# Kernel optimization log

Measured on AMD Instinct MI355X. Metric: run time of the kernel, lower is better.

The kernel has to match this reference:

```python
import jax, jax.numpy as jnp
import numpy as np

FS = 16000
NUM_BANDS = 15
CENTER_FREQ = 150
FFT_SIZE = 512
FFT_IN = 256
HOP = 128
NUM_FRAMES = 30
BETA = 1.0 + 10.0 ** (15.0 / 20.0)
FFT_PAD = (FFT_SIZE - FFT_IN) // 2
ROWS = FFT_SIZE // 2 + 1


def _make_fftmat():
    window = np.hanning(FFT_IN)
    window = np.concatenate([np.zeros(FFT_PAD), window, np.zeros(FFT_PAD)])
    fft = np.fft.fft(np.eye(FFT_SIZE))
    fft = np.vstack((np.real(fft[:ROWS, :]), np.imag(fft[:ROWS, :])))
    fft = window * fft  # (2*ROWS, FFT_SIZE)
    return fft.astype(np.float32)


def _make_octmat(fs=FS, nfft=FFT_SIZE, numBands=NUM_BANDS, mn=CENTER_FREQ):
    f = np.linspace(0, fs, nfft + 1)
    f = f[: int(nfft / 2) + 1]
    k = np.arange(float(numBands))
    cf = 2 ** (k / 3) * mn
    fl = np.sqrt(2.0 ** (k / 3) * mn * 2 ** ((k - 1.0) / 3) * mn)
    fr = np.sqrt(2.0 ** (k / 3) * mn * 2 ** ((k + 1.0) / 3) * mn)
    A = np.zeros((numBands, len(f)))
    for i in range(len(cf)):
        b = np.argmin((f - fl[i]) ** 2)
        fl[i] = f[b]
        fl_ii = b
        b = np.argmin((f - fr[i]) ** 2)
        fr[i] = f[b]
        fr_ii = b
        A[i, np.arange(fl_ii, fr_ii)] = 1
    rnk = np.sum(A, axis=1)
    nb = np.where((rnk[1:] >= rnk[:-1]) & (rnk[1:] != 0))[-1][-1] + 1
    A = A[: nb + 1, :]
    return A.astype(np.float32)


def setup_inputs() -> dict:
    key = jax.random.key(0)
    k1, k2, k3 = jax.random.split(key, 3)
    B, L = 64, 128000
    return {
        "prediction": jax.random.normal(k1, (B, L), dtype=jnp.float32),
        "target": jax.random.normal(k2, (B, L), dtype=jnp.float32),
        "inteference": jax.random.normal(k3, (B, L), dtype=jnp.float32),
        "fftmat": jnp.asarray(_make_fftmat()),   # (514, 512)
        "octmat": jnp.asarray(_make_octmat()),   # (n_bands, 257)
    }


def _stft_mag(seq, fftmat):
    # seq: (B, L) -> conv1d with stride HOP, padding FFT_PAD
    out = jax.lax.conv_general_dilated(
        seq[:, None, :], fftmat[:, None, :],
        window_strides=(HOP,), padding=[(FFT_PAD, FFT_PAD)],
        dimension_numbers=("NCH", "OIH", "NCH"))
    real, imag = out[:, :ROWS, :], out[:, ROWS:, :]
    return jnp.sqrt(real ** 2 + imag ** 2)  # (B, ROWS, T)


def _stoi_loss(prediction, target, fftmat, octmat):
    pred_mag = _stft_mag(prediction, fftmat)
    targ_mag = _stft_mag(target, fftmat)
    # octave-band energies: (B, n_bands, T)
    x = jnp.sqrt(jnp.einsum("bft,kf->bkt", targ_mag ** 2, octmat))
    y = jnp.sqrt(jnp.einsum("bft,kf->bkt", pred_mag ** 2, octmat))
    T = x.shape[2]
    W = T - NUM_FRAMES  # windows for m in [NUM_FRAMES, T)
    idx = jnp.arange(W)[:, None] + jnp.arange(NUM_FRAMES)[None, :]  # (W, 30)
    xw = x[:, :, idx]  # (B, K, W, 30)
    yw = y[:, :, idx]
    alpha = jnp.sqrt(jnp.sum(xw ** 2, axis=3, keepdims=True)
                     / (jnp.sum(yw ** 2, axis=3, keepdims=True) + 1e-07))
    yp = jnp.minimum(alpha * yw, BETA * xw)
    xn = xw - jnp.mean(xw, axis=3, keepdims=True)
    xn = xn / jnp.sqrt(jnp.sum(xn ** 2, axis=3, keepdims=True))
    yn = yp - jnp.mean(yp, axis=3, keepdims=True)
    yn = yn / jnp.sqrt(jnp.sum(yn ** 2, axis=3, keepdims=True))
    # per-window correlation: mean over (B, K) of sum over time
    r = jnp.mean(jnp.sum(xn * yn, axis=3), axis=(0, 1))  # (W,)
    return -jnp.sum(r) / W


def reference(prediction, target, inteference, fftmat, octmat):
    return _stoi_loss(prediction, target, fftmat, octmat)
```

## Files before the change

### kernel.cpp

```cpp
#include <hip/hip_runtime.h>
#include <math.h>

#define SIG_L 128000
#define NBATCH 64
#define NROWS 257
#define HOP 128
#define NUMF 999
#define NFRM 30
#define NWIN 969
#define NB_MAX 16
#define FBINS 160
#define TILES 9
#define KSTEPS 16
#define FPBX 256
#define NTX 4
#define AKB 18432
#define BCH 4112
#define BETA_F 6.623413251903491f

typedef __attribute__((ext_vector_type(8))) short short8;
typedef __attribute__((ext_vector_type(16))) float f32x16;
typedef unsigned short ushort_t;

__device__ inline ushort_t bf_hi_rne(float v, float* rem) {
    unsigned u = __float_as_uint(v);
    unsigned hr = (u + 0x7FFFu + ((u >> 16) & 1u)) & 0xFFFF0000u;
    *rem = v - __uint_as_float(hr);
    return (ushort_t)(hr >> 16);
}
__device__ inline ushort_t bf_rne(float v) {
    unsigned u = __float_as_uint(v);
    return (ushort_t)((u + 0x7FFFu + ((u >> 16) & 1u)) >> 16);
}

__device__ inline void gll16(const void* g, void* l) {
    __builtin_amdgcn_global_load_lds(
        (const __attribute__((address_space(1))) unsigned int*)g,
        (__attribute__((address_space(3))) unsigned int*)l, 16, 0, 0);
}

__global__ void k_scan(const float* __restrict__ oct, int NB, int* __restrict__ hdr) {
    __shared__ int smin[16], smax[16];
    int tid = threadIdx.x;
    if (tid < NB) { smin[tid] = 0x7fffffff; smax[tid] = -1; }
    __syncthreads();
    for (int idx = tid; idx < NB * NROWS; idx += blockDim.x) {
        int k = idx / NROWS, f = idx % NROWS;
        if (oct[idx] != 0.0f) { atomicMin(&smin[k], f); atomicMax(&smax[k], f); }
    }
    __syncthreads();
    if (tid < FBINS) {
        int kid = -1;
        for (int k = 0; k < NB; ++k)
            if (smax[k] >= 0 && tid >= smin[k] && tid <= smax[k]) kid = k;
        hdr[32 + tid] = kid;
    }
}

__global__ void k_prep(const float* __restrict__ fftmat, ushort_t* __restrict__ wpack) {
    for (int u = 0; u < 2; ++u) {
        int idx = blockIdx.x * 512 + u * 256 + threadIdx.x;
        int e = idx & 7, l = (idx >> 3) & 63, p = (idx >> 9) & 1;
        int tt = (idx >> 10) % TILES, kk = (idx >> 10) / TILES;
        int row32 = l & 31, kq = l >> 5;
        int bin = tt * 16 + (row32 >> 1);
        int part = row32 & 1;
        int k = kk * 16 + kq * 8 + e;
        float v = fftmat[(size_t)(part ? (NROWS + bin) : bin) * 512 + 128 + k];
        float rem; ushort_t hb = bf_hi_rne(v, &rem);
        wpack[idx] = p ? bf_rne(rem) : hb;
    }
}

__global__ __launch_bounds__(768, 3) void k_stft(
    const float* __restrict__ targ, const float* __restrict__ pred,
    const ushort_t* __restrict__ wpack, const int* __restrict__ hdr,
    float* __restrict__ xbuf, float* __restrict__ ybuf, int NB) {
    __shared__ __align__(16) char smem[2 * AKB + BCH * 16 + NB_MAX * FPBX * 4 + 640];
    ushort_t* As    = (ushort_t*)smem;
    char*     Bs    = smem + 2 * AKB;
    float*    bacc  = (float*)(smem + 2 * AKB + BCH * 16);
    int*      kmapS = (int*)(smem + 2 * AKB + BCH * 16 + NB_MAX * FPBX * 4);

    const int tid = threadIdx.x;
    const int lane = tid & 63;
    const int wv = __builtin_amdgcn_readfirstlane(tid >> 6);
    const int mg  = wv >> 2;
    const int col = wv & 3;
    const int tbase = mg * 3;
    const int b = blockIdx.y, z = blockIdx.z;
    const int t0 = blockIdx.x * FPBX;
    const float* __restrict__ sig = z ? pred : targ;
    float* __restrict__ out = z ? ybuf : xbuf;
    const size_t boff = (size_t)b * SIG_L;

    for (int i = tid; i < NB_MAX * FPBX; i += 768) bacc[i] = 0.0f;
    for (int i = tid; i < FBINS; i += 768) kmapS[i] = hdr[32 + i];

    const long sbase = (long)t0 * HOP;
    for (int c = tid; c < BCH; c += 768) {
        const long g0 = sbase + (long)c * 8;
        float v[8];
        if (g0 + 8 <= SIG_L) {
            float4 x0 = *(const float4*)(sig + boff + g0);
            float4 x1 = *(const float4*)(sig + boff + g0 + 4);
            v[0] = x0.x; v[1] = x0.y; v[2] = x0.z; v[3] = x0.w;
            v[4] = x1.x; v[5] = x1.y; v[6] = x1.z; v[7] = x1.w;
        } else {
#pragma unroll
            for (int e = 0; e < 8; ++e)
                v[e] = (g0 + e < SIG_L) ? sig[boff + g0 + e] : 0.0f;
        }
        short8 sv;
#pragma unroll
        for (int e = 0; e < 8; ++e) sv[e] = (short)bf_rne(v[e]);
        int byte = c * 16;
        byte ^= ((byte >> 8) & 0xF) << 4;
        *(short8*)(Bs + byte) = sv;
    }
    {
        const char* gsrc = (const char*)wpack;
        for (int j = wv; j < 18; j += 12)
            gll16(gsrc + j * 1024 + lane * 16, smem + j * 1024);
    }
    __syncthreads();

    f32x16 acc[3][2];
#pragma unroll
    for (int g = 0; g < 3; ++g)
#pragma unroll
        for (int bt = 0; bt < 2; ++bt)
#pragma unroll
            for (int e = 0; e < 16; ++e) acc[g][bt][e] = 0.0f;

    const int jloc = lane & 31, kq = lane >> 5;

    int cur = 0;
#pragma unroll 1
    for (int kk = 0; kk < KSTEPS; ++kk) {
        if (kk < KSTEPS - 1) {
            const char* gsrc = (const char*)wpack + (size_t)(kk + 1) * AKB;
            char* ldst = smem + (cur ^ 1) * AKB;
            for (int j = wv; j < 18; j += 12)
                gll16(gsrc + j * 1024 + lane * 16, ldst + j * 1024);
        }
        short8 S[2];
#pragma unroll
        for (int bt = 0; bt < 2; ++bt) {
            const int fl = col * 64 + bt * 32 + jloc;
            int byte = fl * 256 + kk * 32 + kq * 16;
            byte ^= ((byte >> 8) & 0xF) << 4;
            S[bt] = *(const short8*)(Bs + byte);
        }
        const ushort_t* ab = As + cur * (AKB / 2) + tbase * 1024 + lane * 8;
        __builtin_amdgcn_s_setprio(1);
#pragma unroll
        for (int g = 0; g < 3; ++g) {
            short8 Ah = *(const short8*)(ab + g * 1024);
            short8 Al = *(const short8*)(ab + g * 1024 + 512);
            acc[g][0] = __builtin_amdgcn_mfma_f32_32x32x16_bf16(Ah, S[0], acc[g][0], 0, 0, 0);
            acc[g][1] = __builtin_amdgcn_mfma_f32_32x32x16_bf16(Ah, S[1], acc[g][1], 0, 0, 0);
            acc[g][0] = __builtin_amdgcn_mfma_f32_32x32x16_bf16(Al, S[0], acc[g][0], 0, 0, 0);
            acc[g][1] = __builtin_amdgcn_mfma_f32_32x32x16_bf16(Al, S[1], acc[g][1], 0, 0, 0);
        }
        __builtin_amdgcn_s_setprio(0);
        __syncthreads();
        cur ^= 1;
    }

#pragma unroll
    for (int g = 0; g < 3; ++g) {
#pragma unroll
        for (int bt = 0; bt < 2; ++bt) {
            const int fl = col * 64 + bt * 32 + jloc;
            float run = 0.0f; int runk = -1;
#pragma unroll
            for (int rr = 0; rr < 8; ++rr) {
                const int m = (rr & 1) + 4 * (rr >> 1) + 2 * kq;
                const int kid = kmapS[(tbase + g) * 16 + m];
                const float vr = acc[g][bt][rr * 2], vi = acc[g][bt][rr * 2 + 1];
                const float e = vr * vr + vi * vi;
                if (kid != runk) {
                    if (runk >= 0) atomicAdd(&bacc[runk * FPBX + fl], run);
                    run = 0.0f; runk = kid;
                }
                if (kid >= 0) run += e;
            }
            if (runk >= 0) atomicAdd(&bacc[runk * FPBX + fl], run);
        }
    }
    __syncthreads();
    for (int idx = tid; idx < NB * FPBX; idx += 768) {
        int k = idx >> 8, t = idx & (FPBX - 1);
        int tg = t0 + t;
        if (tg < NUMF)
            out[((size_t)b * NB + k) * NUMF + tg] = bacc[k * FPBX + t];
    }
}

__global__ __launch_bounds__(256) void k_corr(const float* __restrict__ xbuf,
                                              const float* __restrict__ ybuf,
                                              int NB, double* __restrict__ partials) {
    const int k = blockIdx.x, b = blockIdx.y;
    const long roff = ((long)b * NB + k) * NUMF;
    __shared__ float xl[NUMF], yl[NUMF];
    __shared__ double red[256];
    const int tid = threadIdx.x;
    for (int i = tid; i < NUMF; i += 256) {
        xl[i] = sqrtf(xbuf[roff + i]);
        yl[i] = sqrtf(ybuf[roff + i]);
    }
    __syncthreads();
    double loc = 0.0;
    for (int w = tid; w < NWIN; w += 256) {
        float sx = 0, sxx = 0, syy = 0;
        for (int i = 0; i < NFRM; ++i) {
            float xv = xl[w + i], yv = yl[w + i];
            sx += xv; sxx += xv * xv; syy += yv * yv;
        }
        float alpha = sqrtf(sxx / (syy + 1e-7f));
        float sy = 0;
        for (int i = 0; i < NFRM; ++i)
            sy += fminf(alpha * yl[w + i], BETA_F * xl[w + i]);
        float mx = sx * (1.0f / NFRM), my = sy * (1.0f / NFRM);
        float cxx = 0, cyy = 0, cxy = 0;
        for (int i = 0; i < NFRM; ++i) {
            float dx = xl[w + i] - mx;
            float dy = fminf(alpha * yl[w + i], BETA_F * xl[w + i]) - my;
            cxx += dx * dx; cyy += dy * dy; cxy += dx * dy;
        }
        loc += (double)cxy / sqrt((double)cxx * (double)cyy);
    }
    red[tid] = loc;
    __syncthreads();
    for (int s = 128; s > 0; s >>= 1) {
        if (tid < s) red[tid] += red[tid + s];
        __syncthreads();
    }
    if (tid == 0) partials[b * NB + k] = red[0];
}

__global__ void k_final(const double* __restrict__ partials, int NB, float* __restrict__ out) {
    __shared__ double red[256];
    const int tid = threadIdx.x;
    const int n = NBATCH * NB;
    double s = 0.0;
    for (int i = tid; i < n; i += 256) s += partials[i];
    red[tid] = s;
    __syncthreads();
    for (int st = 128; st > 0; st >>= 1) {
        if (tid < st) red[tid] += red[tid + st];
        __syncthreads();
    }
    if (tid == 0) out[0] = (float)(-red[0] / ((double)NBATCH * NB * NWIN));
}

extern "C" void kernel_launch(void* const* d_in, const int* in_sizes, int n_in,
                              void* d_out, int out_size, void* d_ws, size_t ws_size,
                              hipStream_t stream) {
    const float* pred   = (const float*)d_in[0];
    const float* targ   = (const float*)d_in[1];
    const float* fftmat = (const float*)d_in[3];
    const float* oct    = (const float*)d_in[4];
    const int NB = in_sizes[4] / NROWS;

    char* ws = (char*)d_ws;
    int*      hdr   = (int*)ws;
    ushort_t* wpack = (ushort_t*)(ws + 1024);
    size_t o1 = 1024 + (size_t)KSTEPS * TILES * 2 * 512 * 2;
    size_t xsz = (size_t)NBATCH * NB_MAX * NUMF * 4;
    float*  xbuf = (float*)(ws + o1);
    float*  ybuf = (float*)(ws + o1 + xsz);
    double* partials = (double*)(ws + o1 + 2 * xsz);

    hipLaunchKernelGGL(k_scan, dim3(1), dim3(256), 0, stream, oct, NB, hdr);
    hipLaunchKernelGGL(k_prep, dim3(288), dim3(256), 0, stream, fftmat, wpack);
    hipLaunchKernelGGL(k_stft, dim3(NTX, NBATCH, 2), dim3(768), 0, stream,
                       targ, pred, wpack, hdr, xbuf, ybuf, NB);
    hipLaunchKernelGGL(k_corr, dim3(NB, NBATCH), dim3(256), 0, stream, xbuf, ybuf, NB, partials);
    hipLaunchKernelGGL(k_final, dim3(1), dim3(256), 0, stream, partials, NB, (float*)d_out);
}
```

Baseline: 103.7 us.

## Make STFT kernel persistent over 256 blocks with batched signal loads

Turns k_stft from a 512-block grid into a 256-block grid where each block loops over two (tile, batch, signal) tasks. It also issues all global signal loads into registers before converting them to bf16, so the loads overlap. A new k_probe kernel with the same shared-memory footprint is launched before k_stft and does no useful work; it looks like a warm-up or timing experiment. The probe adds a launch and extra time to the measured sequence, and halving the block count may reduce parallelism on the device.

```diff
diff --git a/kernel.cpp b/kernel.cpp
--- a/kernel.cpp
+++ b/kernel.cpp
@@ -13,9 +13,9 @@
 #define TILES 9
 #define KSTEPS 16
 #define FPBX 256
-#define NTX 4
 #define AKB 18432
 #define BCH 4112
+#define SMEMSZ (2 * AKB + BCH * 16 + NB_MAX * FPBX * 4 + 640)
 #define BETA_F 6.623413251903491f
 
 typedef __attribute__((ext_vector_type(8))) short short8;
@@ -72,11 +72,22 @@
     }
 }
 
+__global__ __launch_bounds__(768, 3) void k_probe(float* sink) {
+    __shared__ __align__(16) char smem[SMEMSZ];
+    float* bacc = (float*)smem;
+    const int tid = threadIdx.x;
+    for (int i = tid; i < 4096; i += 768) bacc[i] = 0.0f;
+    __syncthreads();
+    float v = bacc[(tid * 37 + 1) & 4095];
+    asm volatile("" :: "v"(v));
+    (void)sink;
+}
+
 __global__ __launch_bounds__(768, 3) void k_stft(
     const float* __restrict__ targ, const float* __restrict__ pred,
     const ushort_t* __restrict__ wpack, const int* __restrict__ hdr,
     float* __restrict__ xbuf, float* __restrict__ ybuf, int NB) {
-    __shared__ __align__(16) char smem[2 * AKB + BCH * 16 + NB_MAX * FPBX * 4 + 640];
+    __shared__ __align__(16) char smem[SMEMSZ];
     ushort_t* As    = (ushort_t*)smem;
     char*     Bs    = smem + 2 * AKB;
     float*    bacc  = (float*)(smem + 2 * AKB + BCH * 16);
@@ -88,113 +99,126 @@
     const int mg  = wv >> 2;
     const int col = wv & 3;
     const int tbase = mg * 3;
-    const int b = blockIdx.y, z = blockIdx.z;
-    const int t0 = blockIdx.x * FPBX;
-    const float* __restrict__ sig = z ? pred : targ;
-    float* __restrict__ out = z ? ybuf : xbuf;
-    const size_t boff = (size_t)b * SIG_L;
-
-    for (int i = tid; i < NB_MAX * FPBX; i += 768) bacc[i] = 0.0f;
+    const int jloc = lane & 31, kq = lane >> 5;
+
     for (int i = tid; i < FBINS; i += 768) kmapS[i] = hdr[32 + i];
 
-    const long sbase = (long)t0 * HOP;
-    for (int c = tid; c < BCH; c += 768) {
-        const long g0 = sbase + (long)c * 8;
-        float v[8];
-        if (g0 + 8 <= SIG_L) {
-            float4 x0 = *(const float4*)(sig + boff + g0);
-            float4 x1 = *(const float4*)(sig + boff + g0 + 4);
-            v[0] = x0.x; v[1] = x0.y; v[2] = x0.z; v[3] = x0.w;
-            v[4] = x1.x; v[5] = x1.y; v[6] = x1.z; v[7] = x1.w;
-        } else {
-#pragma unroll
-            for (int e = 0; e < 8; ++e)
-                v[e] = (g0 + e < SIG_L) ? sig[boff + g0 + e] : 0.0f;
-        }
-        short8 sv;
-#pragma unroll
-        for (int e = 0; e < 8; ++e) sv[e] = (short)bf_rne(v[e]);
-        int byte = c * 16;
-        byte ^= ((byte >> 8) & 0xF) << 4;
-        *(short8*)(Bs + byte) = sv;
-    }
-    {
-        const char* gsrc = (const char*)wpack;
-        for (int j = wv; j < 18; j += 12)
-            gll16(gsrc + j * 1024 + lane * 16, smem + j * 1024);
-    }
-    __syncthreads();
-
-    f32x16 acc[3][2];
-#pragma unroll
-    for (int g = 0; g < 3; ++g)
-#pragma unroll
-        for (int bt = 0; bt < 2; ++bt)
-#pragma unroll
-            for (int e = 0; e < 16; ++e) acc[g][bt][e] = 0.0f;
-
-    const int jloc = lane & 31, kq = lane >> 5;
-
-    int cur = 0;
 #pragma unroll 1
-    for (int kk = 0; kk < KSTEPS; ++kk) {
-        if (kk < KSTEPS - 1) {
-            const char* gsrc = (const char*)wpack + (size_t)(kk + 1) * AKB;
-            char* ldst = smem + (cur ^ 1) * AKB;
+    for (int task = 0; task < 2; ++task) {
+        const int t = (int)blockIdx.x + 256 * task;
+        const int z = t & 1, b = (t >> 1) & 63, tile = (t >> 7) & 3;
+        const int t0 = tile * FPBX;
+        const float* __restrict__ sig = z ? pred : targ;
+        float* __restrict__ out = z ? ybuf : xbuf;
+        const size_t boff = (size_t)b * SIG_L;
+
+        if (task) __syncthreads();
+        for (int i = tid; i < NB_MAX * FPBX; i += 768) bacc[i] = 0.0f;
+
+        const long sbase = (long)t0 * HOP;
+        float4 xr[12];
+#pragma unroll
+        for (int u = 0; u < 6; ++u) {
+            const int c = tid + u * 768;
+            const long g0 = sbase + (long)c * 8;
+            const bool full = (c < BCH) && (g0 + 8 <= SIG_L);
+            const long gc = full ? g0 : 0;
+            const float* p = sig + boff + gc;
+            float4 a0 = *(const float4*)(p);
+            float4 a1 = *(const float4*)(p + 4);
+            if (!full) { a0 = (float4){0,0,0,0}; a1 = (float4){0,0,0,0}; }
+            xr[2*u] = a0; xr[2*u+1] = a1;
+        }
+#pragma unroll
+        for (int u = 0; u < 6; ++u) {
+            const int c = tid + u * 768;
+            if (c < BCH) {
+                short8 sv;
+                sv[0]=(short)bf_rne(xr[2*u].x);   sv[1]=(short)bf_rne(xr[2*u].y);
+                sv[2]=(short)bf_rne(xr[2*u].z);   sv[3]=(short)bf_rne(xr[2*u].w);
+                sv[4]=(short)bf_rne(xr[2*u+1].x); sv[5]=(short)bf_rne(xr[2*u+1].y);
+                sv[6]=(short)bf_rne(xr[2*u+1].z); sv[7]=(short)bf_rne(xr[2*u+1].w);
+                int byte = c * 16;
+                byte ^= ((byte >> 8) & 0xF) << 4;
+                *(short8*)(Bs + byte) = sv;
+            }
+        }
+        {
+            const char* gsrc = (const char*)wpack;
             for (int j = wv; j < 18; j += 12)
-                gll16(gsrc + j * 1024 + lane * 16, ldst + j * 1024);
-        }
-        short8 S[2];
-#pragma unroll
-        for (int bt = 0; bt < 2; ++bt) {
-            const int fl = col * 64 + bt * 32 + jloc;
-            int byte = fl * 256 + kk * 32 + kq * 16;
-            byte ^= ((byte >> 8) & 0xF) << 4;
-            S[bt] = *(const short8*)(Bs + byte);
-        }
-        const ushort_t* ab = As + cur * (AKB / 2) + tbase * 1024 + lane * 8;
-        __builtin_amdgcn_s_setprio(1);
+                gll16(gsrc + j * 1024 + lane * 16, smem + j * 1024);
+        }
+        __syncthreads();
+
+        f32x16 acc[3][2];
+#pragma unroll
+        for (int g = 0; g < 3; ++g)
+#pragma unroll
+            for (int bt = 0; bt < 2; ++bt)
+#pragma unroll
+                for (int e = 0; e < 16; ++e) acc[g][bt][e] = 0.0f;
+
+        int cur = 0;
+#pragma unroll 1
+        for (int kk = 0; kk < KSTEPS; ++kk) {
+            if (kk < KSTEPS - 1) {
+                const char* gsrc = (const char*)wpack + (size_t)(kk + 1) * AKB;
+                char* ldst = smem + (cur ^ 1) * AKB;
+                for (int j = wv; j < 18; j += 12)
+                    gll16(gsrc + j * 1024 + lane * 16, ldst + j * 1024);
+            }
+            short8 S[2];
+#pragma unroll
+            for (int bt = 0; bt < 2; ++bt) {
+                const int fl = col * 64 + bt * 32 + jloc;
+                int byte = fl * 256 + kk * 32 + kq * 16;
+                byte ^= ((byte >> 8) & 0xF) << 4;
+                S[bt] = *(const short8*)(Bs + byte);
+            }
+            const ushort_t* ab = As + cur * (AKB / 2) + tbase * 1024 + lane * 8;
+            __builtin_amdgcn_s_setprio(1);
+#pragma unroll
+            for (int g = 0; g < 3; ++g) {
+                short8 Ah = *(const short8*)(ab + g * 1024);
+                short8 Al = *(const short8*)(ab + g * 1024 + 512);
+                acc[g][0] = __builtin_amdgcn_mfma_f32_32x32x16_bf16(Ah, S[0], acc[g][0], 0, 0, 0);
+                acc[g][1] = __builtin_amdgcn_mfma_f32_32x32x16_bf16(Ah, S[1], acc[g][1], 0, 0, 0);
+                acc[g][0] = __builtin_amdgcn_mfma_f32_32x32x16_bf16(Al, S[0], acc[g][0], 0, 0, 0);
+                acc[g][1] = __builtin_amdgcn_mfma_f32_32x32x16_bf16(Al, S[1], acc[g][1], 0, 0, 0);
+            }
+            __builtin_amdgcn_s_setprio(0);
+            __syncthreads();
+            cur ^= 1;
+        }
+
 #pragma unroll
         for (int g = 0; g < 3; ++g) {
-            short8 Ah = *(const short8*)(ab + g * 1024);
-            short8 Al = *(const short8*)(ab + g * 1024 + 512);
-            acc[g][0] = __builtin_amdgcn_mfma_f32_32x32x16_bf16(Ah, S[0], acc[g][0], 0, 0, 0);
-            acc[g][1] = __builtin_amdgcn_mfma_f32_32x32x16_bf16(Ah, S[1], acc[g][1], 0, 0, 0);
-            acc[g][0] = __builtin_amdgcn_mfma_f32_32x32x16_bf16(Al, S[0], acc[g][0], 0, 0, 0);
-            acc[g][1] = __builtin_amdgcn_mfma_f32_32x32x16_bf16(Al, S[1], acc[g][1], 0, 0, 0);
-        }
-        __builtin_amdgcn_s_setprio(0);
+#pragma unroll
+            for (int bt = 0; bt < 2; ++bt) {
+                const int fl = col * 64 + bt * 32 + jloc;
+                float run = 0.0f; int runk = -1;
+#pragma unroll
+                for (int rr = 0; rr < 8; ++rr) {
+                    const int m = (rr & 1) + 4 * (rr >> 1) + 2 * kq;
+                    const int kid = kmapS[(tbase + g) * 16 + m];
+                    const float vr = acc[g][bt][rr * 2], vi = acc[g][bt][rr * 2 + 1];
+                    const float e = vr * vr + vi * vi;
+                    if (kid != runk) {
+                        if (runk >= 0) atomicAdd(&bacc[runk * FPBX + fl], run);
+                        run = 0.0f; runk = kid;
+                    }
+                    if (kid >= 0) run += e;
+                }
+                if (runk >= 0) atomicAdd(&bacc[runk * FPBX + fl], run);
+            }
+        }
         __syncthreads();
-        cur ^= 1;
-    }
-
-#pragma unroll
-    for (int g = 0; g < 3; ++g) {
-#pragma unroll
-        for (int bt = 0; bt < 2; ++bt) {
-            const int fl = col * 64 + bt * 32 + jloc;
-            float run = 0.0f; int runk = -1;
-#pragma unroll
-            for (int rr = 0; rr < 8; ++rr) {
-                const int m = (rr & 1) + 4 * (rr >> 1) + 2 * kq;
-                const int kid = kmapS[(tbase + g) * 16 + m];
-                const float vr = acc[g][bt][rr * 2], vi = acc[g][bt][rr * 2 + 1];
-                const float e = vr * vr + vi * vi;
-                if (kid != runk) {
-                    if (runk >= 0) atomicAdd(&bacc[runk * FPBX + fl], run);
-                    run = 0.0f; runk = kid;
-                }
-                if (kid >= 0) run += e;
-            }
-            if (runk >= 0) atomicAdd(&bacc[runk * FPBX + fl], run);
-        }
-    }
-    __syncthreads();
-    for (int idx = tid; idx < NB * FPBX; idx += 768) {
-        int k = idx >> 8, t = idx & (FPBX - 1);
-        int tg = t0 + t;
-        if (tg < NUMF)
-            out[((size_t)b * NB + k) * NUMF + tg] = bacc[k * FPBX + t];
+        for (int idx = tid; idx < NB * FPBX; idx += 768) {
+            int k = idx >> 8, tt = idx & (FPBX - 1);
+            int tg = t0 + tt;
+            if (tg < NUMF)
+                out[((size_t)b * NB + k) * NUMF + tg] = bacc[k * FPBX + tt];
+        }
     }
 }
 
@@ -275,7 +299,8 @@
 
     hipLaunchKernelGGL(k_scan, dim3(1), dim3(256), 0, stream, oct, NB, hdr);
     hipLaunchKernelGGL(k_prep, dim3(288), dim3(256), 0, stream, fftmat, wpack);
-    hipLaunchKernelGGL(k_stft, dim3(NTX, NBATCH, 2), dim3(768), 0, stream,
+    hipLaunchKernelGGL(k_probe, dim3(512), dim3(768), 0, stream, xbuf);
+    hipLaunchKernelGGL(k_stft, dim3(256), dim3(768), 0, stream,
                        targ, pred, wpack, hdr, xbuf, ybuf, NB);
     hipLaunchKernelGGL(k_corr, dim3(NB, NBATCH), dim3(256), 0, stream, xbuf, ybuf, NB, partials);
     hipLaunchKernelGGL(k_final, dim3(1), dim3(256), 0, stream, partials, NB, (float*)d_out);
```

Measured after the change: 105.7 us. About the same (+1.9%).
